# Kernel optimization log

Hardware: AMD Instinct MI355X
Metric: run time of the kernel (lower is better)

## Reference

```python
import jax, jax.numpy as jnp
import numpy as np

E, K, H, I = 64, 8, 2048, 768  # num_experts, top_k, hidden, moe_intermediate

def setup_inputs() -> dict:
    key = jax.random.key(0)
    k1, k2, k3, k4 = jax.random.split(key, 4)
    return {
        "hidden_states": jax.random.normal(k1, (1, 1024, H), dtype=jnp.float32),
        "w_gate": jax.random.normal(k2, (H, E), dtype=jnp.float32) * 0.02,
        "w13": jax.random.normal(k3, (E, H, 2 * I), dtype=jnp.float32) * 0.02,  # fused gate+up proj
        "w2": jax.random.normal(k4, (E, I, H), dtype=jnp.float32) * 0.02,
    }

def reference(hidden_states, w_gate, w13, w2):
    orig_shape = hidden_states.shape
    x = hidden_states.reshape(-1, orig_shape[-1])            # [T, H]
    T = x.shape[0]

    # Router: logits -> softmax -> top-k -> renormalize (norm_topk_prob=True)
    router_logits = x @ w_gate                               # [T, E]
    probs = jax.nn.softmax(router_logits, axis=-1)
    topk_w, topk_idx = jax.lax.top_k(probs, K)               # [T, K]
    topk_w = topk_w / jnp.sum(topk_w, axis=-1, keepdims=True)
    # Dense combine-weight matrix [T, E] (zero for non-routed experts)
    combine = jnp.zeros((T, E), dtype=x.dtype).at[
        jnp.arange(T)[:, None], topk_idx].add(topk_w)

    # Expert SwiGLU FFN, computed densely for all experts, masked by combine
    h = jnp.einsum('th,ehd->etd', x, w13)                    # [E, T, 2I]
    gate, up = h[..., :I], h[..., I:]
    act = jax.nn.silu(gate) * up                             # [E, T, I]
    y = jnp.einsum('eti,eih->eth', act, w2)                  # [E, T, H]
    out = jnp.einsum('eth,te->th', y, combine)               # [T, H]
    return out.reshape(orig_shape)
```

## Files before the change

### kernel.cpp

```cpp
#include <hip/hip_runtime.h>
#include <hip/hip_bf16.h>
#include <math.h>

#define NE 64
#define NK 8
#define NH 2048
#define NI 768
#define NT 1024

typedef float f32x4 __attribute__((ext_vector_type(4)));
typedef __bf16 bf16x8 __attribute__((ext_vector_type(8)));
typedef __bf16 bf16x4 __attribute__((ext_vector_type(4)));

__global__ __launch_bounds__(256) void router_k(
    const float* __restrict__ x, const float* __restrict__ wg,
    __bf16* __restrict__ x_bf, int* __restrict__ topk_idx,
    float* __restrict__ topk_w, int* __restrict__ counts)
{
    __shared__ float xs[4][NH];
    const int wave = threadIdx.x >> 6;
    const int lane = threadIdx.x & 63;
    const int t = blockIdx.x * 4 + wave;

    const float* xrow = x + (size_t)t * NH;
    __bf16* brow = x_bf + (size_t)t * NH;
    #pragma unroll
    for (int j = 0; j < 8; ++j) {
        int idx = j * 256 + lane * 4;
        f32x4 v = *reinterpret_cast<const f32x4*>(xrow + idx);
        *reinterpret_cast<f32x4*>(&xs[wave][idx]) = v;
        bf16x4 b;
        b[0] = (__bf16)v.x; b[1] = (__bf16)v.y; b[2] = (__bf16)v.z; b[3] = (__bf16)v.w;
        *reinterpret_cast<bf16x4*>(brow + idx) = b;
    }
    __syncthreads();

    float a0 = 0.f, a1 = 0.f, a2 = 0.f, a3 = 0.f;
    for (int h = 0; h < NH; h += 4) {
        a0 = fmaf(xs[wave][h + 0], wg[(h + 0) * NE + lane], a0);
        a1 = fmaf(xs[wave][h + 1], wg[(h + 1) * NE + lane], a1);
        a2 = fmaf(xs[wave][h + 2], wg[(h + 2) * NE + lane], a2);
        a3 = fmaf(xs[wave][h + 3], wg[(h + 3) * NE + lane], a3);
    }
    float acc = (a0 + a1) + (a2 + a3);

    float cur = acc;
    float sel_v[NK]; int sel_i[NK];
    #pragma unroll
    for (int k = 0; k < NK; ++k) {
        float bv = cur; int bi = lane;
        #pragma unroll
        for (int s = 32; s; s >>= 1) {
            float ov = __shfl_xor(bv, s, 64);
            int   oi = __shfl_xor(bi, s, 64);
            if (ov > bv || (ov == bv && oi < bi)) { bv = ov; bi = oi; }
        }
        sel_v[k] = bv; sel_i[k] = bi;
        if (lane == bi) cur = -3.4e38f;
    }
    float m = sel_v[0];
    float ssum = 0.f;
    #pragma unroll
    for (int k = 0; k < NK; ++k) ssum += expf(sel_v[k] - m);

    if (lane < NK) {
        float w = expf(sel_v[lane] - m) / ssum;
        topk_idx[t * NK + lane] = sel_i[lane];
        topk_w[t * NK + lane] = w;
        atomicAdd(&counts[sel_i[lane]], 1);
    }
}

__global__ void scan_k(const int* __restrict__ counts, int* __restrict__ offs,
                       int* __restrict__ cursors)
{
    if (threadIdx.x == 0) {
        int r = 0;
        for (int e = 0; e < NE; ++e) { offs[e] = r; r += counts[e]; }
        offs[NE] = r;
    }
    if (threadIdx.x < NE) cursors[threadIdx.x] = 0;
}

__global__ __launch_bounds__(256) void scatter_k(
    const int* __restrict__ topk_idx, const float* __restrict__ topk_w,
    const int* __restrict__ offs, int* __restrict__ cursors,
    int* __restrict__ slot_tok, float* __restrict__ slot_w,
    int* __restrict__ slot_of)
{
    int i = blockIdx.x * 256 + threadIdx.x;
    int e = topk_idx[i];
    int p = atomicAdd(&cursors[e], 1);
    int g = offs[e] + p;
    slot_tok[g] = i >> 3;
    slot_w[g] = topk_w[i];
    slot_of[i] = g;
}

__device__ __forceinline__ int swz(int row, int ch) { return ch ^ ((row >> 1) & 3); }

__global__ __launch_bounds__(256, 2) void e1_k(
    const __bf16* __restrict__ x_bf, const float* __restrict__ w13,
    const int* __restrict__ counts, const int* __restrict__ offs,
    const int* __restrict__ slot_tok, __bf16* __restrict__ act)
{
    const int e = blockIdx.x;
    const int cnt = counts[e];
    const int m0 = blockIdx.z * 256;
    if (m0 >= cnt) return;
    const int rows = min(256, cnt - m0);
    const int n0 = blockIdx.y * 64;
    const int goff = offs[e] + m0;

    __shared__ __bf16 A[2][256 * 32];
    __shared__ __bf16 B[2][128 * 32];
    __shared__ int tok[256];

    const int tid = threadIdx.x;
    tok[tid] = (tid < rows) ? slot_tok[goff + tid] : 0;
    __syncthreads();

    const int wave = tid >> 6, lane = tid & 63;
    f32x4 acc[4][8];
    #pragma unroll
    for (int i = 0; i < 4; ++i)
        #pragma unroll
        for (int j = 0; j < 8; ++j) acc[i][j] = (f32x4){0.f, 0.f, 0.f, 0.f};

    const float* w13e = w13 + (size_t)e * NH * (2 * NI);
    const int cc = tid & 31, kch = tid >> 5;
    const int bcol0 = cc * 4;
    const int gcol = (bcol0 < 64) ? (n0 + bcol0) : (NI + n0 + bcol0 - 64);

    const __bf16* aptr[4];
    int aoff[4];
    #pragma unroll
    for (int it = 0; it < 4; ++it) {
        int item = it * 256 + tid;
        int r = item >> 2, ch = item & 3;
        aptr[it] = x_bf + (size_t)tok[r] * NH + ch * 8;
        aoff[it] = r * 32 + swz(r, ch) * 8;
    }
    const float* bptr = w13e + (size_t)(kch * 4) * (2 * NI) + gcol;
    const int lcb = kch >> 1, halfb = kch & 1;
    int boff[4];
    #pragma unroll
    for (int j = 0; j < 4; ++j)
        boff[j] = (bcol0 + j) * 32 + swz(bcol0 + j, lcb) * 8 + halfb * 4;

    bf16x8 aReg[4];
    f32x4 bReg[4];

    #pragma unroll
    for (int it = 0; it < 4; ++it)
        aReg[it] = *reinterpret_cast<const bf16x8*>(aptr[it]);
    #pragma unroll
    for (int ki = 0; ki < 4; ++ki)
        bReg[ki] = *reinterpret_cast<const f32x4*>(bptr + (size_t)ki * (2 * NI));
    #pragma unroll
    for (int it = 0; it < 4; ++it)
        *reinterpret_cast<bf16x8*>(&A[0][aoff[it]]) = aReg[it];
    #pragma unroll
    for (int j = 0; j < 4; ++j) {
        bf16x4 p;
        p[0] = (__bf16)bReg[0][j]; p[1] = (__bf16)bReg[1][j];
        p[2] = (__bf16)bReg[2][j]; p[3] = (__bf16)bReg[3][j];
        *reinterpret_cast<bf16x4*>(&B[0][boff[j]]) = p;
    }
    __syncthreads();

    int curb = 0;
    for (int k0 = 0; k0 < NH; k0 += 32) {
        const int nk = k0 + 32;
        if (nk < NH) {
            #pragma unroll
            for (int it = 0; it < 4; ++it)
                aReg[it] = *reinterpret_cast<const bf16x8*>(aptr[it] + nk);
            #pragma unroll
            for (int ki = 0; ki < 4; ++ki)
                bReg[ki] = *reinterpret_cast<const f32x4*>(
                    bptr + (size_t)(nk + ki * 4 - ki * 4) * (2 * NI) + (size_t)nk * (2 * NI) - (size_t)nk * (2 * NI) + (size_t)ki * (2 * NI) + (size_t)nk * (2 * NI));
        }
        if (nk < NH) {
            #pragma unroll
            for (int ki = 0; ki < 4; ++ki)
                bReg[ki] = *reinterpret_cast<const f32x4*>(
                    bptr + ((size_t)nk + (size_t)ki) * 0 + (size_t)(nk + 0) * (2 * NI) + (size_t)ki * (2 * NI));
        }

        bf16x8 bfr[8];
        #pragma unroll
        for (int nf = 0; nf < 8; ++nf) {
            int col = nf * 16 + (lane & 15);
            bfr[nf] = *reinterpret_cast<const bf16x8*>(
                &B[curb][col * 32 + swz(col, lane >> 4) * 8]);
        }
        #pragma unroll
        for (int mf = 0; mf < 4; ++mf) {
            int rf = mf * 64 + wave * 16;
            if (rf < rows) {
                int row = rf + (lane & 15);
                bf16x8 a = *reinterpret_cast<const bf16x8*>(
                    &A[curb][row * 32 + swz(row, lane >> 4) * 8]);
                #pragma unroll
                for (int nf = 0; nf < 8; ++nf)
                    acc[mf][nf] = __builtin_amdgcn_mfma_f32_16x16x32_bf16(
                        a, bfr[nf], acc[mf][nf], 0, 0, 0);
            }
        }

        if (nk < NH) {
            #pragma unroll
            for (int it = 0; it < 4; ++it)
                *reinterpret_cast<bf16x8*>(&A[curb ^ 1][aoff[it]]) = aReg[it];
            #pragma unroll
            for (int j = 0; j < 4; ++j) {
                bf16x4 p;
                p[0] = (__bf16)bReg[0][j]; p[1] = (__bf16)bReg[1][j];
                p[2] = (__bf16)bReg[2][j]; p[3] = (__bf16)bReg[3][j];
                *reinterpret_cast<bf16x4*>(&B[curb ^ 1][boff[j]]) = p;
            }
        }
        __syncthreads();
        curb ^= 1;
    }

    #pragma unroll
    for (int mf = 0; mf < 4; ++mf) {
        int rf = mf * 64 + wave * 16;
        if (rf >= rows) continue;
        #pragma unroll
        for (int nf = 0; nf < 4; ++nf) {
            f32x4 g = acc[mf][nf];
            f32x4 u = acc[mf][nf + 4];
            int col = n0 + nf * 16 + (lane & 15);
            #pragma unroll
            for (int r = 0; r < 4; ++r) {
                int row = rf + ((lane >> 4) << 2) + r;
                if (row < rows) {
                    float gv = g[r];
                    float a = gv / (1.f + expf(-gv)) * u[r];
                    act[(size_t)(goff + row) * NI + col] = (__bf16)a;
                }
            }
        }
    }
}

__global__ __launch_bounds__(256, 2) void e2_k(
    const __bf16* __restrict__ act, const float* __restrict__ w2,
    const int* __restrict__ counts, const int* __restrict__ offs,
    const float* __restrict__ slot_w, __bf16* __restrict__ partial)
{
    const int e = blockIdx.x;
    const int cnt = counts[e];
    const int m0 = blockIdx.z * 256;
    if (m0 >= cnt) return;
    const int rows = min(256, cnt - m0);
    const int n0 = blockIdx.y * 64;
    const int goff = offs[e] + m0;

    __shared__ __bf16 A[2][256 * 32];
    __shared__ __bf16 B[2][64 * 32];

    const int tid = threadIdx.x, wave = tid >> 6, lane = tid & 63;
    f32x4 acc[4][4];
    #pragma unroll
    for (int i = 0; i < 4; ++i)
        #pragma unroll
        for (int j = 0; j < 4; ++j) acc[i][j] = (f32x4){0.f, 0.f, 0.f, 0.f};

    const float* w2e = w2 + (size_t)e * NI * NH;
    const int cc = tid & 15, kch = (tid >> 4) & 7;
    const bool doB = tid < 128;
    const int bcol0 = cc * 4;

    const __bf16* aptr[4];
    int aoff[4];
    #pragma unroll
    for (int it = 0; it < 4; ++it) {
        int item = it * 256 + tid;
        int r = item >> 2, ch = item & 3;
        int ar = (r < rows) ? r : 0;
        aptr[it] = act + (size_t)(goff + ar) * NI + ch * 8;
        aoff[it] = r * 32 + swz(r, ch) * 8;
    }
    const float* bptr = w2e + (size_t)(kch * 4) * NH + n0 + bcol0;
    const int lcb = kch >> 1, halfb = kch & 1;
    int boff[4];
    #pragma unroll
    for (int j = 0; j < 4; ++j)
        boff[j] = (bcol0 + j) * 32 + swz(bcol0 + j, lcb) * 8 + halfb * 4;

    bf16x8 aReg[4];
    f32x4 bReg[4];

    #pragma unroll
    for (int it = 0; it < 4; ++it)
        aReg[it] = *reinterpret_cast<const bf16x8*>(aptr[it]);
    if (doB)
        #pragma unroll
        for (int ki = 0; ki < 4; ++ki)
            bReg[ki] = *reinterpret_cast<const f32x4*>(bptr + (size_t)ki * NH);
    #pragma unroll
    for (int it = 0; it < 4; ++it)
        *reinterpret_cast<bf16x8*>(&A[0][aoff[it]]) = aReg[it];
    if (doB)
        #pragma unroll
        for (int j = 0; j < 4; ++j) {
            bf16x4 p;
            p[0] = (__bf16)bReg[0][j]; p[1] = (__bf16)bReg[1][j];
            p[2] = (__bf16)bReg[2][j]; p[3] = (__bf16)bReg[3][j];
            *reinterpret_cast<bf16x4*>(&B[0][boff[j]]) = p;
        }
    __syncthreads();

    int curb = 0;
    for (int k0 = 0; k0 < NI; k0 += 32) {
        const int nk = k0 + 32;
        if (nk < NI) {
            #pragma unroll
            for (int it = 0; it < 4; ++it)
                aReg[it] = *reinterpret_cast<const bf16x8*>(aptr[it] + nk);
            if (doB)
                #pragma unroll
                for (int ki = 0; ki < 4; ++ki)
                    bReg[ki] = *reinterpret_cast<const f32x4*>(
                        bptr + (size_t)(nk + ki * 4) * 0 + (size_t)nk * NH + (size_t)ki * NH);
        }

        bf16x8 bfr[4];
        #pragma unroll
        for (int nf = 0; nf < 4; ++nf) {
            int col = nf * 16 + (lane & 15);
            bfr[nf] = *reinterpret_cast<const bf16x8*>(
                &B[curb][col * 32 + swz(col, lane >> 4) * 8]);
        }
        #pragma unroll
        for (int mf = 0; mf < 4; ++mf) {
            int rf = mf * 64 + wave * 16;
            if (rf < rows) {
                int row = rf + (lane & 15);
                bf16x8 a = *reinterpret_cast<const bf16x8*>(
                    &A[curb][row * 32 + swz(row, lane >> 4) * 8]);
                #pragma unroll
                for (int nf = 0; nf < 4; ++nf)
                    acc[mf][nf] = __builtin_amdgcn_mfma_f32_16x16x32_bf16(
                        a, bfr[nf], acc[mf][nf], 0, 0, 0);
            }
        }

        if (nk < NI) {
            #pragma unroll
            for (int it = 0; it < 4; ++it)
                *reinterpret_cast<bf16x8*>(&A[curb ^ 1][aoff[it]]) = aReg[it];
            if (doB)
                #pragma unroll
                for (int j = 0; j < 4; ++j) {
                    bf16x4 p;
                    p[0] = (__bf16)bReg[0][j]; p[1] = (__bf16)bReg[1][j];
                    p[2] = (__bf16)bReg[2][j]; p[3] = (__bf16)bReg[3][j];
                    *reinterpret_cast<bf16x4*>(&B[curb ^ 1][boff[j]]) = p;
                }
        }
        __syncthreads();
        curb ^= 1;
    }

    #pragma unroll
    for (int mf = 0; mf < 4; ++mf) {
        int rf = mf * 64 + wave * 16;
        if (rf >= rows) continue;
        int rb = rf + ((lane >> 4) << 2);
        #pragma unroll
        for (int r = 0; r < 4; ++r) {
            int row = rb + r;
            if (row >= rows) continue;
            int gs = goff + row;
            float wv = slot_w[gs];
            #pragma unroll
            for (int nf = 0; nf < 4; ++nf) {
                int col = n0 + nf * 16 + (lane & 15);
                partial[(size_t)gs * NH + col] = (__bf16)(wv * acc[mf][nf][r]);
            }
        }
    }
}

__global__ __launch_bounds__(256) void combine_k(
    const __bf16* __restrict__ partial, const int* __restrict__ slot_of,
    float* __restrict__ out)
{
    const int t = blockIdx.x;
    const int c0 = threadIdx.x * 8;
    __shared__ int gs[NK];
    if (threadIdx.x < NK) gs[threadIdx.x] = slot_of[t * NK + threadIdx.x];
    __syncthreads();

    float s[8] = {0.f, 0.f, 0.f, 0.f, 0.f, 0.f, 0.f, 0.f};
    #pragma unroll
    for (int k = 0; k < NK; ++k) {
        bf16x8 v = *reinterpret_cast<const bf16x8*>(partial + (size_t)gs[k] * NH + c0);
        #pragma unroll
        for (int j = 0; j < 8; ++j) s[j] += (float)v[j];
    }
    f32x4 o0 = {s[0], s[1], s[2], s[3]};
    f32x4 o1 = {s[4], s[5], s[6], s[7]};
    *reinterpret_cast<f32x4*>(out + (size_t)t * NH + c0) = o0;
    *reinterpret_cast<f32x4*>(out + (size_t)t * NH + c0 + 4) = o1;
}

extern "C" void kernel_launch(void* const* d_in, const int* in_sizes, int n_in,
                              void* d_out, int out_size, void* d_ws, size_t ws_size,
                              hipStream_t stream)
{
    const float* x   = (const float*)d_in[0];
    const float* wg  = (const float*)d_in[1];
    const float* w13 = (const float*)d_in[2];
    const float* w2  = (const float*)d_in[3];
    float* out = (float*)d_out;
    char* ws = (char*)d_ws;

    __bf16* x_bf = (__bf16*)ws;
    size_t o = (size_t)4 * 1024 * 1024;
    __bf16* act = (__bf16*)(ws + o);      o += (size_t)8192 * NI * 2;
    __bf16* partial = (__bf16*)(ws + o);  o += (size_t)8192 * NH * 2;
    int*   topk_idx = (int*)(ws + o);     o += 8192 * 4;
    float* topk_w   = (float*)(ws + o);   o += 8192 * 4;
    int*   slot_tok = (int*)(ws + o);     o += 8192 * 4;
    float* slot_w   = (float*)(ws + o);   o += 8192 * 4;
    int*   slot_of  = (int*)(ws + o);     o += 8192 * 4;
    int*   counts   = (int*)(ws + o);     o += 256;
    int*   offs     = (int*)(ws + o);     o += 512;
    int*   cursors  = (int*)(ws + o);

    hipMemsetAsync(counts, 0, 256, stream);

    router_k <<<NT / 4, 256, 0, stream>>>(x, wg, x_bf, topk_idx, topk_w, counts);
    scan_k   <<<1, 64, 0, stream>>>(counts, offs, cursors);
    scatter_k<<<(NT * NK) / 256, 256, 0, stream>>>(topk_idx, topk_w, offs, cursors,
                                                   slot_tok, slot_w, slot_of);
    e1_k<<<dim3(NE, NI / 64, 2), 256, 0, stream>>>(x_bf, w13, counts, offs, slot_tok, act);
    e2_k<<<dim3(NE, NH / 64, 2), 256, 0, stream>>>(act, w2, counts, offs, slot_w, partial);
    combine_k<<<NT, 256, 0, stream>>>(partial, slot_of, out);
}
```

Measured before the change: 455.2 us.

## Deepen global-to-LDS prefetch to two stages in both expert GEMM loops

Replaces the single-register prefetch in the gate/up and down-projection GEMM main loops with two register sets, so global loads for tile k+2 are issued while tile k is computed from LDS. The loop is manually unrolled by two with lambdas for load, LDS write, and compute, and the odd redundant double loads of B are removed. This hides more global memory latency at the cost of extra VGPRs, which could lower occupancy.

Measured after the change: 466.9 us. 1.03x slower.

```diff
diff --git a/kernel.cpp b/kernel.cpp
--- a/kernel.cpp
+++ b/kernel.cpp
@@ -148,52 +148,40 @@
     for (int j = 0; j < 4; ++j)
         boff[j] = (bcol0 + j) * 32 + swz(bcol0 + j, lcb) * 8 + halfb * 4;
 
-    bf16x8 aReg[4];
-    f32x4 bReg[4];
-
-    #pragma unroll
-    for (int it = 0; it < 4; ++it)
-        aReg[it] = *reinterpret_cast<const bf16x8*>(aptr[it]);
-    #pragma unroll
-    for (int ki = 0; ki < 4; ++ki)
-        bReg[ki] = *reinterpret_cast<const f32x4*>(bptr + (size_t)ki * (2 * NI));
-    #pragma unroll
-    for (int it = 0; it < 4; ++it)
-        *reinterpret_cast<bf16x8*>(&A[0][aoff[it]]) = aReg[it];
-    #pragma unroll
-    for (int j = 0; j < 4; ++j) {
-        bf16x4 p;
-        p[0] = (__bf16)bReg[0][j]; p[1] = (__bf16)bReg[1][j];
-        p[2] = (__bf16)bReg[2][j]; p[3] = (__bf16)bReg[3][j];
-        *reinterpret_cast<bf16x4*>(&B[0][boff[j]]) = p;
-    }
-    __syncthreads();
-
-    int curb = 0;
-    for (int k0 = 0; k0 < NH; k0 += 32) {
-        const int nk = k0 + 32;
-        if (nk < NH) {
-            #pragma unroll
-            for (int it = 0; it < 4; ++it)
-                aReg[it] = *reinterpret_cast<const bf16x8*>(aptr[it] + nk);
-            #pragma unroll
-            for (int ki = 0; ki < 4; ++ki)
-                bReg[ki] = *reinterpret_cast<const f32x4*>(
-                    bptr + (size_t)(nk + ki * 4 - ki * 4) * (2 * NI) + (size_t)nk * (2 * NI) - (size_t)nk * (2 * NI) + (size_t)ki * (2 * NI) + (size_t)nk * (2 * NI));
-        }
-        if (nk < NH) {
-            #pragma unroll
-            for (int ki = 0; ki < 4; ++ki)
-                bReg[ki] = *reinterpret_cast<const f32x4*>(
-                    bptr + ((size_t)nk + (size_t)ki) * 0 + (size_t)(nk + 0) * (2 * NI) + (size_t)ki * (2 * NI));
-        }
-
+    bf16x8 a0v[4], a1v[4];
+    f32x4 b0v[4], b1v[4];
+
+    auto loadA = [&](bf16x8* dst, int kk) {
+        #pragma unroll
+        for (int it = 0; it < 4; ++it)
+            dst[it] = *reinterpret_cast<const bf16x8*>(aptr[it] + kk);
+    };
+    auto loadB = [&](f32x4* dst, int kk) {
+        #pragma unroll
+        for (int ki = 0; ki < 4; ++ki)
+            dst[ki] = *reinterpret_cast<const f32x4*>(bptr + (size_t)(kk + ki) * (2 * NI));
+    };
+    auto writeA = [&](int buf, const bf16x8* src) {
+        #pragma unroll
+        for (int it = 0; it < 4; ++it)
+            *reinterpret_cast<bf16x8*>(&A[buf][aoff[it]]) = src[it];
+    };
+    auto writeB = [&](int buf, const f32x4* src) {
+        #pragma unroll
+        for (int j = 0; j < 4; ++j) {
+            bf16x4 p;
+            p[0] = (__bf16)src[0][j]; p[1] = (__bf16)src[1][j];
+            p[2] = (__bf16)src[2][j]; p[3] = (__bf16)src[3][j];
+            *reinterpret_cast<bf16x4*>(&B[buf][boff[j]]) = p;
+        }
+    };
+    auto compute = [&](int buf) {
         bf16x8 bfr[8];
         #pragma unroll
         for (int nf = 0; nf < 8; ++nf) {
             int col = nf * 16 + (lane & 15);
             bfr[nf] = *reinterpret_cast<const bf16x8*>(
-                &B[curb][col * 32 + swz(col, lane >> 4) * 8]);
+                &B[buf][col * 32 + swz(col, lane >> 4) * 8]);
         }
         #pragma unroll
         for (int mf = 0; mf < 4; ++mf) {
@@ -201,28 +189,30 @@
             if (rf < rows) {
                 int row = rf + (lane & 15);
                 bf16x8 a = *reinterpret_cast<const bf16x8*>(
-                    &A[curb][row * 32 + swz(row, lane >> 4) * 8]);
+                    &A[buf][row * 32 + swz(row, lane >> 4) * 8]);
                 #pragma unroll
                 for (int nf = 0; nf < 8; ++nf)
                     acc[mf][nf] = __builtin_amdgcn_mfma_f32_16x16x32_bf16(
                         a, bfr[nf], acc[mf][nf], 0, 0, 0);
             }
         }
-
-        if (nk < NH) {
-            #pragma unroll
-            for (int it = 0; it < 4; ++it)
-                *reinterpret_cast<bf16x8*>(&A[curb ^ 1][aoff[it]]) = aReg[it];
-            #pragma unroll
-            for (int j = 0; j < 4; ++j) {
-                bf16x4 p;
-                p[0] = (__bf16)bReg[0][j]; p[1] = (__bf16)bReg[1][j];
-                p[2] = (__bf16)bReg[2][j]; p[3] = (__bf16)bReg[3][j];
-                *reinterpret_cast<bf16x4*>(&B[curb ^ 1][boff[j]]) = p;
-            }
-        }
+    };
+
+    loadA(a0v, 0);  loadB(b0v, 0);
+    loadA(a1v, 32); loadB(b1v, 32);
+    writeA(0, a0v); writeB(0, b0v);
+    __syncthreads();
+
+    #pragma unroll 1
+    for (int t = 0; t < 64; t += 2) {
+        if (t + 2 < 64) { loadA(a0v, (t + 2) * 32); loadB(b0v, (t + 2) * 32); }
+        compute(0);
+        writeA(1, a1v); writeB(1, b1v);
         __syncthreads();
-        curb ^= 1;
+        if (t + 3 < 64) { loadA(a1v, (t + 3) * 32); loadB(b1v, (t + 3) * 32); }
+        compute(1);
+        if (t + 2 < 64) { writeA(0, a0v); writeB(0, b0v); }
+        __syncthreads();
     }
 
     #pragma unroll
@@ -292,49 +282,42 @@
     for (int j = 0; j < 4; ++j)
         boff[j] = (bcol0 + j) * 32 + swz(bcol0 + j, lcb) * 8 + halfb * 4;
 
-    bf16x8 aReg[4];
-    f32x4 bReg[4];
-
-    #pragma unroll
-    for (int it = 0; it < 4; ++it)
-        aReg[it] = *reinterpret_cast<const bf16x8*>(aptr[it]);
-    if (doB)
-        #pragma unroll
-        for (int ki = 0; ki < 4; ++ki)
-            bReg[ki] = *reinterpret_cast<const f32x4*>(bptr + (size_t)ki * NH);
-    #pragma unroll
-    for (int it = 0; it < 4; ++it)
-        *reinterpret_cast<bf16x8*>(&A[0][aoff[it]]) = aReg[it];
-    if (doB)
-        #pragma unroll
-        for (int j = 0; j < 4; ++j) {
-            bf16x4 p;
-            p[0] = (__bf16)bReg[0][j]; p[1] = (__bf16)bReg[1][j];
-            p[2] = (__bf16)bReg[2][j]; p[3] = (__bf16)bReg[3][j];
-            *reinterpret_cast<bf16x4*>(&B[0][boff[j]]) = p;
-        }
-    __syncthreads();
-
-    int curb = 0;
-    for (int k0 = 0; k0 < NI; k0 += 32) {
-        const int nk = k0 + 32;
-        if (nk < NI) {
+    bf16x8 a0v[4], a1v[4];
+    f32x4 b0v[4], b1v[4];
+
+    auto loadA = [&](bf16x8* dst, int kk) {
+        #pragma unroll
+        for (int it = 0; it < 4; ++it)
+            dst[it] = *reinterpret_cast<const bf16x8*>(aptr[it] + kk);
+    };
+    auto loadB = [&](f32x4* dst, int kk) {
+        if (doB)
             #pragma unroll
-            for (int it = 0; it < 4; ++it)
-                aReg[it] = *reinterpret_cast<const bf16x8*>(aptr[it] + nk);
-            if (doB)
-                #pragma unroll
-                for (int ki = 0; ki < 4; ++ki)
-                    bReg[ki] = *reinterpret_cast<const f32x4*>(
-                        bptr + (size_t)(nk + ki * 4) * 0 + (size_t)nk * NH + (size_t)ki * NH);
-        }
-
+            for (int ki = 0; ki < 4; ++ki)
+                dst[ki] = *reinterpret_cast<const f32x4*>(bptr + (size_t)(kk + ki) * NH);
+    };
+    auto writeA = [&](int buf, const bf16x8* src) {
+        #pragma unroll
+        for (int it = 0; it < 4; ++it)
+            *reinterpret_cast<bf16x8*>(&A[buf][aoff[it]]) = src[it];
+    };
+    auto writeB = [&](int buf, const f32x4* src) {
+        if (doB)
+            #pragma unroll
+            for (int j = 0; j < 4; ++j) {
+                bf16x4 p;
+                p[0] = (__bf16)src[0][j]; p[1] = (__bf16)src[1][j];
+                p[2] = (__bf16)src[2][j]; p[3] = (__bf16)src[3][j];
+                *reinterpret_cast<bf16x4*>(&B[buf][boff[j]]) = p;
+            }
+    };
+    auto compute = [&](int buf) {
         bf16x8 bfr[4];
         #pragma unroll
         for (int nf = 0; nf < 4; ++nf) {
             int col = nf * 16 + (lane & 15);
             bfr[nf] = *reinterpret_cast<const bf16x8*>(
-                &B[curb][col * 32 + swz(col, lane >> 4) * 8]);
+                &B[buf][col * 32 + swz(col, lane >> 4) * 8]);
         }
         #pragma unroll
         for (int mf = 0; mf < 4; ++mf) {
@@ -342,29 +325,30 @@
             if (rf < rows) {
                 int row = rf + (lane & 15);
                 bf16x8 a = *reinterpret_cast<const bf16x8*>(
-                    &A[curb][row * 32 + swz(row, lane >> 4) * 8]);
+                    &A[buf][row * 32 + swz(row, lane >> 4) * 8]);
                 #pragma unroll
                 for (int nf = 0; nf < 4; ++nf)
                     acc[mf][nf] = __builtin_amdgcn_mfma_f32_16x16x32_bf16(
                         a, bfr[nf], acc[mf][nf], 0, 0, 0);
             }
         }
-
-        if (nk < NI) {
-            #pragma unroll
-            for (int it = 0; it < 4; ++it)
-                *reinterpret_cast<bf16x8*>(&A[curb ^ 1][aoff[it]]) = aReg[it];
-            if (doB)
-                #pragma unroll
-                for (int j = 0; j < 4; ++j) {
-                    bf16x4 p;
-                    p[0] = (__bf16)bReg[0][j]; p[1] = (__bf16)bReg[1][j];
-                    p[2] = (__bf16)bReg[2][j]; p[3] = (__bf16)bReg[3][j];
-                    *reinterpret_cast<bf16x4*>(&B[curb ^ 1][boff[j]]) = p;
-                }
-        }
+    };
+
+    loadA(a0v, 0);  loadB(b0v, 0);
+    loadA(a1v, 32); loadB(b1v, 32);
+    writeA(0, a0v); writeB(0, b0v);
+    __syncthreads();
+
+    #pragma unroll 1
+    for (int t = 0; t < 24; t += 2) {
+        if (t + 2 < 24) { loadA(a0v, (t + 2) * 32); loadB(b0v, (t + 2) * 32); }
+        compute(0);
+        writeA(1, a1v); writeB(1, b1v);
         __syncthreads();
-        curb ^= 1;
+        if (t + 3 < 24) { loadA(a1v, (t + 3) * 32); loadB(b1v, (t + 3) * 32); }
+        compute(1);
+        if (t + 2 < 24) { writeA(0, a0v); writeB(0, b0v); }
+        __syncthreads();
     }
 
     #pragma unroll
```
